# Kernel tuning notes

Hardware: AMD Instinct MI355X
Metric: run time of the kernel (lower is better)

The kernel has to match this reference:

```python
import jax, jax.numpy as jnp
import numpy as np

N_NODES = 50000
N_EDGES = 800000
H = 128
IN_DIM = 512
N_LAYERS = 3
LN_EPS = 1e-5


def setup_inputs() -> dict:
    key = jax.random.key(0)
    ks = jax.random.split(key, 12)
    s_in = 1.0 / np.sqrt(IN_DIM)
    s_h = 1.0 / np.sqrt(H)
    return {
        "peptide_feature": jax.random.normal(ks[0], (N_NODES, IN_DIM), jnp.float32),
        "proj_W": jax.random.uniform(ks[1], (IN_DIM, H), jnp.float32, -s_in, s_in),
        "proj_b": jax.random.uniform(ks[2], (H,), jnp.float32, -s_in, s_in),
        "edge_emb": jax.random.normal(ks[3], (100, H), jnp.float32),
        "conv_W1": jax.random.uniform(ks[4], (N_LAYERS, H, H), jnp.float32, -s_h, s_h),
        "conv_b1": jax.random.uniform(ks[5], (N_LAYERS, H), jnp.float32, -s_h, s_h),
        "conv_W2": jax.random.uniform(ks[6], (N_LAYERS, H, H), jnp.float32, -s_h, s_h),
        "conv_b2": jax.random.uniform(ks[7], (N_LAYERS, H), jnp.float32, -s_h, s_h),
        "ln_gamma": jnp.ones((H,), jnp.float32),
        "ln_beta": jnp.zeros((H,), jnp.float32),
        "edge_index": jax.random.randint(ks[8], (2, N_EDGES), 0, N_NODES, jnp.int64 if jax.config.jax_enable_x64 else jnp.int32),
        "edge_attr": jax.random.randint(ks[9], (N_EDGES, 1), 0, 100, jnp.int64 if jax.config.jax_enable_x64 else jnp.int32),
    }


def reference(peptide_feature, proj_W, proj_b, edge_emb, conv_W1, conv_b1,
              conv_W2, conv_b2, ln_gamma, ln_beta, edge_index, edge_attr):
    # aanet_proj: Linear(512, H)
    x = peptide_feature @ proj_W + proj_b  # [N, H]
    # edge type embedding lookup
    ea = edge_emb[edge_attr[:, 0]]  # [E, H]
    src, dst = edge_index[0], edge_index[1]
    n = x.shape[0]
    for i in range(N_LAYERS):
        # GINEConv (eps=0): aggr_i = sum_{(j->i)} relu(x_j + e_ji); out = MLP(x + aggr)
        msg = jax.nn.relu(x[src] + ea)  # [E, H] gather + add + relu
        agg = jax.ops.segment_sum(msg, dst, num_segments=n)  # scatter-add [N, H]
        h = x + agg
        h = jax.nn.relu(h @ conv_W1[i] + conv_b1[i]) @ conv_W2[i] + conv_b2[i]
        x = h + x  # residual
    # LayerNorm over last dim
    mu = jnp.mean(x, axis=-1, keepdims=True)
    var = jnp.var(x, axis=-1, keepdims=True)
    return ln_gamma * (x - mu) * jax.lax.rsqrt(var + LN_EPS) + ln_beta
```

## Files before the change

kernel.cpp:

```cpp
#include <hip/hip_runtime.h>
#include <hip/hip_bf16.h>

#define N_NODES 50000
#define N_EDGES 800000
#define H 128
#define IN_DIM 512
#define N_LAYERS 3
#define LN_EPS 1e-5f
#define SCAN_B ((N_NODES + 255) / 256)
#define BIN_CH 8192
#define BIN_BLOCKS ((N_EDGES + BIN_CH - 1) / BIN_CH)

typedef __attribute__((ext_vector_type(4))) float f32x4;
typedef __attribute__((ext_vector_type(8))) short short8;

__device__ inline ushort f2bfu(float f) {
    __hip_bfloat16 h = __float2bfloat16(f);
    return __builtin_bit_cast(ushort, h);
}
__device__ inline float bfu2f(ushort u) {
    uint v = ((uint)u) << 16;
    return __builtin_bit_cast(float, v);
}
__device__ inline float lobf(uint u) { return __builtin_bit_cast(float, u << 16); }
__device__ inline float hibf(uint u) { return __builtin_bit_cast(float, u & 0xffff0000u); }

#define SWZ(row, byte) ((byte) ^ (((row) & 7) << 4))

__device__ inline short8 cvt8(float4 a, float4 b) {
    short8 v;
    v[0] = (short)f2bfu(a.x); v[1] = (short)f2bfu(a.y);
    v[2] = (short)f2bfu(a.z); v[3] = (short)f2bfu(a.w);
    v[4] = (short)f2bfu(b.x); v[5] = (short)f2bfu(b.y);
    v[6] = (short)f2bfu(b.z); v[7] = (short)f2bfu(b.w);
    return v;
}


__global__ __launch_bounds__(256) void bucketcnt_k(const int* __restrict__ dst,
                                                   int* __restrict__ bcnt) {
    __shared__ int cnt[SCAN_B];
    int tid = threadIdx.x;
    if (tid < SCAN_B) cnt[tid] = 0;
    __syncthreads();
    int e0 = blockIdx.x * BIN_CH;
    #pragma unroll
    for (int k = 0; k < BIN_CH / 256; k++) {
        int e = e0 + k * 256 + tid;
        if (e < N_EDGES) atomicAdd(&cnt[dst[e] >> 8], 1);
    }
    __syncthreads();
    if (tid < SCAN_B && cnt[tid] > 0) atomicAdd(&bcnt[tid], cnt[tid]);
}

__global__ __launch_bounds__(256) void scanb_k(const int* __restrict__ bcnt,
                                               int* __restrict__ bbase,
                                               int* __restrict__ bcur) {
    __shared__ int s[256];
    int t = threadIdx.x;
    int v = (t < SCAN_B) ? bcnt[t] : 0;
    s[t] = v;
    __syncthreads();
    for (int d = 1; d < 256; d <<= 1) {
        int u = (t >= d) ? s[t - d] : 0;
        __syncthreads();
        s[t] += u;
        __syncthreads();
    }
    int exc = s[t] - v;
    bbase[t] = exc;
    if (t < SCAN_B) bcur[t] = exc;
}


__global__ __launch_bounds__(256) void binpass_k(const int* __restrict__ src,
                                                 const int* __restrict__ dst,
                                                 const int* __restrict__ attr,
                                                 int* __restrict__ bcur,
                                                 int* __restrict__ tmp_ep,
                                                 ushort* __restrict__ tmp_dst) {
    __shared__ int cnt[SCAN_B];
    __shared__ int lofs[SCAN_B];
    __shared__ int gbase[SCAN_B];
    __shared__ int cnt2[SCAN_B];
    __shared__ int scan_s[256];
    __shared__ int stage_ep[BIN_CH];
    __shared__ ushort stage_dst[BIN_CH];
    int tid = threadIdx.x;
    int e0 = blockIdx.x * BIN_CH;

    if (tid < SCAN_B) { cnt[tid] = 0; cnt2[tid] = 0; }
    __syncthreads();

    #pragma unroll
    for (int k = 0; k < BIN_CH / 256; k++) {
        int e = e0 + k * 256 + tid;
        if (e < N_EDGES) atomicAdd(&cnt[dst[e] >> 8], 1);
    }
    __syncthreads();

    int v = (tid < SCAN_B) ? cnt[tid] : 0;
    scan_s[tid] = v;
    __syncthreads();
    for (int d = 1; d < 256; d <<= 1) {
        int u = (tid >= d) ? scan_s[tid - d] : 0;
        __syncthreads();
        scan_s[tid] += u;
        __syncthreads();
    }
    if (tid < SCAN_B) lofs[tid] = scan_s[tid] - v;
    int total = scan_s[255];

    if (tid < SCAN_B && v > 0) gbase[tid] = atomicAdd(&bcur[tid], v);
    __syncthreads();

    #pragma unroll
    for (int k = 0; k < BIN_CH / 256; k++) {
        int e = e0 + k * 256 + tid;
        if (e < N_EDGES) {
            int d = dst[e];
            int b = d >> 8;
            int loc = lofs[b] + atomicAdd(&cnt2[b], 1);
            stage_ep[loc] = src[e] | (attr[e] << 16);
            stage_dst[loc] = (ushort)d;
        }
    }
    __syncthreads();

    for (int i = tid; i < total; i += 256) {
        ushort d = stage_dst[i];
        int b = d >> 8;
        int gp = gbase[b] + (i - lofs[b]);
        tmp_ep[gp] = stage_ep[i];
        tmp_dst[gp] = d;
    }
}


__global__ __launch_bounds__(256) void finepass_k(const int* __restrict__ tmp_ep,
                                                  const ushort* __restrict__ tmp_dst,
                                                  const int* __restrict__ bbase,
                                                  int* __restrict__ offs,
                                                  int* __restrict__ epack) {
    __shared__ int deg[256];
    __shared__ int cur[256];
    __shared__ int wsum[4];
    int tid = threadIdx.x;
    deg[tid] = 0;
    __syncthreads();
    int lo = bbase[blockIdx.x], hi = bbase[blockIdx.x + 1];
    for (int i = lo + tid; i < hi; i += 256)
        atomicAdd(&deg[tmp_dst[i] & 255], 1);
    __syncthreads();
    int lane = tid & 63, w = tid >> 6;
    int v = deg[tid];
    int inc = v;
    #pragma unroll
    for (int d = 1; d < 64; d <<= 1) {
        int u = __shfl_up(inc, d);
        if (lane >= d) inc += u;
    }
    if (lane == 63) wsum[w] = inc;
    __syncthreads();
    int wo = 0;
    #pragma unroll
    for (int k = 0; k < 4; k++) if (k < w) wo += wsum[k];
    int exc = lo + wo + inc - v;
    int node = (blockIdx.x << 8) + tid;
    if (node < N_NODES) offs[node] = exc;
    if (node == N_NODES - 1) offs[N_NODES] = exc + v;
    cur[tid] = exc;
    __syncthreads();
    for (int i = lo + tid; i < hi; i += 256) {
        ushort d = tmp_dst[i];
        int ep = tmp_ep[i];
        int pos = atomicAdd(&cur[d & 255], 1);
        epack[pos] = ep;
    }
}


__global__ __launch_bounds__(256) void prep_w_k(const float* __restrict__ pW,
                                                const float* __restrict__ W1,
                                                const float* __restrict__ W2,
                                                const float* __restrict__ emb,
                                                short* __restrict__ Wt,
                                                short* __restrict__ W1t,
                                                short* __restrict__ W2t,
                                                ushort* __restrict__ embb,
                                                int* __restrict__ bcnt) {
    int i = blockIdx.x * 256 + threadIdx.x;
    if (i < 128 * 512) {
        int n = i >> 9, k = i & 511;
        Wt[i] = (short)f2bfu(pW[k * 128 + n]);
    }
    if (i < 3 * 128 * 128) {
        int l = i >> 14, rem = i & 16383, n = rem >> 7, k = rem & 127;
        W1t[i] = (short)f2bfu(W1[l * 16384 + k * 128 + n]);
        W2t[i] = (short)f2bfu(W2[l * 16384 + k * 128 + n]);
    }
    if (i < 100 * 128) embb[i] = f2bfu(emb[i]);
    if (i < 256) bcnt[i] = 0;
}


__global__ __launch_bounds__(512) void proj_k(const float* __restrict__ pep,
                                              const short* __restrict__ Wt,
                                              const float* __restrict__ b,
                                              float* __restrict__ xf,
                                              ushort* __restrict__ xb) {
    __shared__ short SW[128 * 512];
    int tid = threadIdx.x, lane = tid & 63, wid = tid >> 6;

    #pragma unroll
    for (int c = 0; c < 16; c++) {
        int ch = tid + c * 512;
        int row = ch >> 6, kc = (ch & 63) * 16;
        short8 w = *(const short8*)((const char*)Wt + row * 1024 + kc);
        *(short8*)((char*)SW + SWZ(row, row * 1024 + kc)) = w;
    }
    __syncthreads();

    int m0 = blockIdx.x * 256 + wid * 32;

    const float* arow[2];
    #pragma unroll
    for (int mi = 0; mi < 2; mi++) {
        int node = m0 + mi * 16 + (lane & 15);
        if (node > N_NODES - 1) node = N_NODES - 1;
        arow[mi] = pep + (size_t)node * IN_DIM + ((lane >> 4) << 3);
    }

    f32x4 acc[2][8] = {};
    float4 A[4][2][2];
    #pragma unroll
    for (int d = 0; d < 4; d++)
        #pragma unroll
        for (int mi = 0; mi < 2; mi++) {
            A[d][mi][0] = *(const float4*)(arow[mi] + d * 32);
            A[d][mi][1] = *(const float4*)(arow[mi] + d * 32 + 4);
        }

    #pragma unroll
    for (int ks = 0; ks < 16; ks++) {
        int d = ks & 3;
        short8 af0 = cvt8(A[d][0][0], A[d][0][1]);
        short8 af1 = cvt8(A[d][1][0], A[d][1][1]);
        if (ks + 4 < 16) {
            #pragma unroll
            for (int mi = 0; mi < 2; mi++) {
                A[d][mi][0] = *(const float4*)(arow[mi] + (ks + 4) * 32);
                A[d][mi][1] = *(const float4*)(arow[mi] + (ks + 4) * 32 + 4);
            }
        }
        int kb2 = (ks * 32 + ((lane >> 4) << 3)) * 2;
        #pragma unroll
        for (int ni = 0; ni < 8; ni++) {
            int n = ni * 16 + (lane & 15);
            short8 bf = *(const short8*)((const char*)SW + SWZ(n, n * 1024 + kb2));
            acc[0][ni] = __builtin_amdgcn_mfma_f32_16x16x32_bf16(af0, bf, acc[0][ni], 0, 0, 0);
            acc[1][ni] = __builtin_amdgcn_mfma_f32_16x16x32_bf16(af1, bf, acc[1][ni], 0, 0, 0);
        }
    }

    #pragma unroll
    for (int ni = 0; ni < 8; ni++) {
        int col = ni * 16 + (lane & 15);
        float bb = b[col];
        #pragma unroll
        for (int mi = 0; mi < 2; mi++) {
            int rowb = m0 + mi * 16 + ((lane >> 4) << 2);
            #pragma unroll
            for (int r = 0; r < 4; r++) {
                int node = rowb + r;
                if (node < N_NODES) {
                    float v = acc[mi][ni][r] + bb;
                    xf[(size_t)node * H + col] = v;
                    xb[(size_t)node * H + col] = f2bfu(v);
                }
            }
        }
    }
}


__global__ __launch_bounds__(256) void gather_k(const ushort* __restrict__ xb,
                                                const int* __restrict__ offs,
                                                const int* __restrict__ epack,
                                                const ushort* __restrict__ embb,
                                                ushort* __restrict__ aggb) {
    int node = (blockIdx.x * 256 + threadIdx.x) >> 6;
    int lane = threadIdx.x & 63;
    if (node >= N_NODES) return;
    int beg = offs[node], end = offs[node + 1];
    float ax = 0.f, ay = 0.f;
    for (int base = beg; base < end; base += 64) {
        int myp = (base + lane < end) ? epack[base + lane] : 0;
        int cnt = min(64, end - base);
        int j = 0;
        for (; j + 4 <= cnt; j += 4) {
            int p0 = __shfl(myp, j), p1 = __shfl(myp, j + 1);
            int p2 = __shfl(myp, j + 2), p3 = __shfl(myp, j + 3);
            uint x0 = *(const uint*)(xb + (size_t)(p0 & 0xffff) * H + lane * 2);
            uint e0 = *(const uint*)(embb + (size_t)(p0 >> 16) * H + lane * 2);
            uint x1 = *(const uint*)(xb + (size_t)(p1 & 0xffff) * H + lane * 2);
            uint e1 = *(const uint*)(embb + (size_t)(p1 >> 16) * H + lane * 2);
            uint x2 = *(const uint*)(xb + (size_t)(p2 & 0xffff) * H + lane * 2);
            uint e2 = *(const uint*)(embb + (size_t)(p2 >> 16) * H + lane * 2);
            uint x3 = *(const uint*)(xb + (size_t)(p3 & 0xffff) * H + lane * 2);
            uint e3 = *(const uint*)(embb + (size_t)(p3 >> 16) * H + lane * 2);
            ax += fmaxf(lobf(x0) + lobf(e0), 0.f);
            ay += fmaxf(hibf(x0) + hibf(e0), 0.f);
            ax += fmaxf(lobf(x1) + lobf(e1), 0.f);
            ay += fmaxf(hibf(x1) + hibf(e1), 0.f);
            ax += fmaxf(lobf(x2) + lobf(e2), 0.f);
            ay += fmaxf(hibf(x2) + hibf(e2), 0.f);
            ax += fmaxf(lobf(x3) + lobf(e3), 0.f);
            ay += fmaxf(hibf(x3) + hibf(e3), 0.f);
        }
        for (; j < cnt; j++) {
            int p = __shfl(myp, j);
            uint xv = *(const uint*)(xb + (size_t)(p & 0xffff) * H + lane * 2);
            uint ev = *(const uint*)(embb + (size_t)(p >> 16) * H + lane * 2);
            ax += fmaxf(lobf(xv) + lobf(ev), 0.f);
            ay += fmaxf(hibf(xv) + hibf(ev), 0.f);
        }
    }
    uint packed = (uint)f2bfu(ax) | ((uint)f2bfu(ay) << 16);
    *(uint*)(aggb + (size_t)node * H + lane * 2) = packed;
}


#define MLP_ROWS 64
__global__ __launch_bounds__(256) void mlp_k(float* __restrict__ xf,
                                             ushort* __restrict__ xb,
                                             const ushort* __restrict__ aggb,
                                             const short* __restrict__ W1t,
                                             const float* __restrict__ b1,
                                             const short* __restrict__ W2t,
                                             const float* __restrict__ b2,
                                             const float* __restrict__ gamma,
                                             const float* __restrict__ beta,
                                             float* __restrict__ out,
                                             int write_xb, int do_ln) {
    __shared__ short S[MLP_ROWS * 128];
    __shared__ short Wb[128 * 128];
    int tid = threadIdx.x, lane = tid & 63, wid = tid >> 6;
    int wr = wid >> 1, wc = wid & 1;
    int m0 = blockIdx.x * MLP_ROWS;

    #pragma unroll
    for (int c = 0; c < 4; c++) {
        int ch = tid + c * 256;
        int row = ch >> 4, k8 = (ch & 15) * 8;
        int node = m0 + row;
        short8 hv;
        if (node < N_NODES) {
            const float* xp = xf + (size_t)node * H + k8;
            float4 x0 = *(const float4*)xp;
            float4 x1 = *(const float4*)(xp + 4);
            short8 ag = *(const short8*)(aggb + (size_t)node * H + k8);
            hv[0] = (short)f2bfu(x0.x + bfu2f((ushort)ag[0]));
            hv[1] = (short)f2bfu(x0.y + bfu2f((ushort)ag[1]));
            hv[2] = (short)f2bfu(x0.z + bfu2f((ushort)ag[2]));
            hv[3] = (short)f2bfu(x0.w + bfu2f((ushort)ag[3]));
            hv[4] = (short)f2bfu(x1.x + bfu2f((ushort)ag[4]));
            hv[5] = (short)f2bfu(x1.y + bfu2f((ushort)ag[5]));
            hv[6] = (short)f2bfu(x1.z + bfu2f((ushort)ag[6]));
            hv[7] = (short)f2bfu(x1.w + bfu2f((ushort)ag[7]));
        } else {
            hv = (short8)0;
        }
        *(short8*)((char*)S + SWZ(row, row * 256 + k8 * 2)) = hv;
    }
    #pragma unroll
    for (int c = 0; c < 8; c++) {
        int ch = tid + c * 256;
        int row = ch >> 4, k8 = (ch & 15) * 8;
        short8 w = *(const short8*)(W1t + row * H + k8);
        *(short8*)((char*)Wb + SWZ(row, row * 256 + k8 * 2)) = w;
    }
    short8 wreg2[8];
    #pragma unroll
    for (int c = 0; c < 8; c++) {
        int ch = tid + c * 256;
        int row = ch >> 4, k8 = (ch & 15) * 8;
        wreg2[c] = *(const short8*)(W2t + row * H + k8);
    }
    __syncthreads();

    f32x4 a1[2][4] = {};
    #pragma unroll
    for (int ks = 0; ks < 4; ks++) {
        int kb = ks * 32 + (lane >> 4) * 8;
        short8 af[2], bfr[4];
        #pragma unroll
        for (int mi = 0; mi < 2; mi++) {
            int r = wr * 32 + mi * 16 + (lane & 15);
            af[mi] = *(const short8*)((const char*)S + SWZ(r, r * 256 + kb * 2));
        }
        #pragma unroll
        for (int ni = 0; ni < 4; ni++) {
            int n = wc * 64 + ni * 16 + (lane & 15);
            bfr[ni] = *(const short8*)((const char*)Wb + SWZ(n, n * 256 + kb * 2));
        }
        #pragma unroll
        for (int mi = 0; mi < 2; mi++)
            #pragma unroll
            for (int ni = 0; ni < 4; ni++)
                a1[mi][ni] = __builtin_amdgcn_mfma_f32_16x16x32_bf16(
                    af[mi], bfr[ni], a1[mi][ni], 0, 0, 0);
    }
    __syncthreads();

    #pragma unroll
    for (int ni = 0; ni < 4; ni++) {
        int n = wc * 64 + ni * 16 + (lane & 15);
        float bb = b1[n];
        #pragma unroll
        for (int mi = 0; mi < 2; mi++) {
            int mrow = wr * 32 + mi * 16 + ((lane >> 4) << 2);
            #pragma unroll
            for (int r = 0; r < 4; r++) {
                int m = mrow + r;
                float tv = fmaxf(a1[mi][ni][r] + bb, 0.f);
                *(ushort*)((char*)S + SWZ(m, m * 256 + n * 2)) = f2bfu(tv);
            }
        }
    }
    #pragma unroll
    for (int c = 0; c < 8; c++) {
        int ch = tid + c * 256;
        int row = ch >> 4, k8 = (ch & 15) * 8;
        *(short8*)((char*)Wb + SWZ(row, row * 256 + k8 * 2)) = wreg2[c];
    }
    __syncthreads();

    f32x4 a2[4][2] = {};
    #pragma unroll
    for (int ks = 0; ks < 4; ks++) {
        int kb = ks * 32 + (lane >> 4) * 8;
        short8 af[4], bfr[2];
        #pragma unroll
        for (int mi = 0; mi < 4; mi++) {
            int n2 = wr * 64 + mi * 16 + (lane & 15);
            af[mi] = *(const short8*)((const char*)Wb + SWZ(n2, n2 * 256 + kb * 2));
        }
        #pragma unroll
        for (int ni = 0; ni < 2; ni++) {
            int m = wc * 32 + ni * 16 + (lane & 15);
            bfr[ni] = *(const short8*)((const char*)S + SWZ(m, m * 256 + kb * 2));
        }
        #pragma unroll
        for (int mi = 0; mi < 4; mi++)
            #pragma unroll
            for (int ni = 0; ni < 2; ni++)
                a2[mi][ni] = __builtin_amdgcn_mfma_f32_16x16x32_bf16(
                    af[mi], bfr[ni], a2[mi][ni], 0, 0, 0);
    }

    if (!do_ln) {
        #pragma unroll
        for (int ni = 0; ni < 2; ni++) {
            int node = m0 + wc * 32 + ni * 16 + (lane & 15);
            if (node >= N_NODES) continue;
            #pragma unroll
            for (int mi = 0; mi < 4; mi++) {
                int n2b = wr * 64 + mi * 16 + ((lane >> 4) << 2);
                float4 xo = *(float4*)(xf + (size_t)node * H + n2b);
                float4 bb = *(const float4*)(b2 + n2b);
                float4 o;
                o.x = a2[mi][ni][0] + bb.x + xo.x;
                o.y = a2[mi][ni][1] + bb.y + xo.y;
                o.z = a2[mi][ni][2] + bb.z + xo.z;
                o.w = a2[mi][ni][3] + bb.w + xo.w;
                *(float4*)(xf + (size_t)node * H + n2b) = o;
                if (write_xb) {
                    ushort us[4] = {f2bfu(o.x), f2bfu(o.y), f2bfu(o.z), f2bfu(o.w)};
                    *(ulong*)(xb + (size_t)node * H + n2b) = *(ulong*)us;
                }
            }
        }
    } else {
        float* F = (float*)Wb;
        __syncthreads();
        #pragma unroll
        for (int ni = 0; ni < 2; ni++) {
            int nl = wc * 32 + ni * 16 + (lane & 15);
            int node = m0 + nl;
            #pragma unroll
            for (int mi = 0; mi < 4; mi++) {
                int n2b = wr * 64 + mi * 16 + ((lane >> 4) << 2);
                float4 o = {0.f, 0.f, 0.f, 0.f};
                if (node < N_NODES) {
                    float4 xo = *(float4*)(xf + (size_t)node * H + n2b);
                    float4 bb = *(const float4*)(b2 + n2b);
                    o.x = a2[mi][ni][0] + bb.x + xo.x;
                    o.y = a2[mi][ni][1] + bb.y + xo.y;
                    o.z = a2[mi][ni][2] + bb.z + xo.z;
                    o.w = a2[mi][ni][3] + bb.w + xo.w;
                }
                *(float4*)((char*)F + SWZ(nl, nl * 512 + n2b * 4)) = o;
            }
        }
        __syncthreads();
        float2 gm = ((const float2*)gamma)[lane];
        float2 bt = ((const float2*)beta)[lane];
        for (int i = 0; i < 16; i++) {
            int row = wid * 16 + i;
            int node = m0 + row;
            if (node >= N_NODES) break;
            float2 v = *(float2*)((char*)F + SWZ(row, row * 512 + lane * 8));
            float s = v.x + v.y;
            #pragma unroll
            for (int d = 1; d < 64; d <<= 1) s += __shfl_xor(s, d);
            float mu = s * (1.f / 128.f);
            float dx = v.x - mu, dy = v.y - mu;
            float q = dx * dx + dy * dy;
            #pragma unroll
            for (int d = 1; d < 64; d <<= 1) q += __shfl_xor(q, d);
            float inv = rsqrtf(q * (1.f / 128.f) + LN_EPS);
            float2 o2;
            o2.x = gm.x * dx * inv + bt.x;
            o2.y = gm.y * dy * inv + bt.y;
            ((float2*)(out + (size_t)node * H))[lane] = o2;
        }
    }
}


extern "C" void kernel_launch(void* const* d_in, const int* in_sizes, int n_in,
                              void* d_out, int out_size, void* d_ws, size_t ws_size,
                              hipStream_t stream) {
    const float* pep    = (const float*)d_in[0];
    const float* proj_W = (const float*)d_in[1];
    const float* proj_b = (const float*)d_in[2];
    const float* emb    = (const float*)d_in[3];
    const float* cW1    = (const float*)d_in[4];
    const float* cb1    = (const float*)d_in[5];
    const float* cW2    = (const float*)d_in[6];
    const float* cb2    = (const float*)d_in[7];
    const float* gamma  = (const float*)d_in[8];
    const float* beta   = (const float*)d_in[9];
    const int*   eidx   = (const int*)d_in[10];
    const int*   attr   = (const int*)d_in[11];
    const int* src = eidx;
    const int* dst = eidx + N_EDGES;

    char* w = (char*)d_ws;
    float*  xf    = (float*)w;              w += (size_t)N_NODES * H * 4;
    ushort* xb    = (ushort*)w;             w += (size_t)N_NODES * H * 2;
    ushort* aggb  = (ushort*)w;             w += (size_t)N_NODES * H * 2;
    short*  Wt    = (short*)w;              w += 128 * 512 * 2;
    short*  W1t   = (short*)w;              w += 3 * 128 * 128 * 2;
    short*  W2t   = (short*)w;              w += 3 * 128 * 128 * 2;
    ushort* embb  = (ushort*)w;             w += 100 * 128 * 2;
    int*    offs  = (int*)w;                w += (N_NODES + 16) * 4;
    int*    bcnt  = (int*)w;                w += 256 * 4;
    int*    bbase = (int*)w;                w += 260 * 4;
    int*    bcur  = (int*)w;                w += 256 * 4;
    int*    epack = (int*)w;                w += (size_t)N_EDGES * 4;
    int*    tmp_ep = (int*)w;               w += (size_t)N_EDGES * 4;
    ushort* tmp_dst = (ushort*)w;           w += (size_t)N_EDGES * 2;

    float* out = (float*)d_out;

    prep_w_k<<<256, 256, 0, stream>>>(proj_W, cW1, cW2, emb, Wt, W1t, W2t, embb, bcnt);
    bucketcnt_k<<<BIN_BLOCKS, 256, 0, stream>>>(dst, bcnt);
    scanb_k<<<1, 256, 0, stream>>>(bcnt, bbase, bcur);
    binpass_k<<<BIN_BLOCKS, 256, 0, stream>>>(src, dst, attr, bcur, tmp_ep, tmp_dst);
    finepass_k<<<SCAN_B, 256, 0, stream>>>(tmp_ep, tmp_dst, bbase, offs, epack);

    proj_k<<<(N_NODES + 255) / 256, 512, 0, stream>>>(pep, Wt, proj_b, xf, xb);

    for (int l = 0; l < N_LAYERS; l++) {
        gather_k<<<(N_NODES * 64 + 255) / 256, 256, 0, stream>>>(
            xb, offs, epack, embb, aggb);
        mlp_k<<<(N_NODES + MLP_ROWS - 1) / MLP_ROWS, 256, 0, stream>>>(
            xf, xb, aggb,
            W1t + (size_t)l * H * H, cb1 + (size_t)l * H,
            W2t + (size_t)l * H * H, cb2 + (size_t)l * H,
            gamma, beta, out,
            (l < N_LAYERS - 1) ? 1 : 0,
            (l == N_LAYERS - 1) ? 1 : 0);
    }
}
```

Before: 277.4 us.

## Fuse CSR build into one persistent kernel with grid barriers, unroll gather

```diff
diff --git a/kernel.cpp b/kernel.cpp
--- a/kernel.cpp
+++ b/kernel.cpp
@@ -8,8 +8,7 @@
 #define N_LAYERS 3
 #define LN_EPS 1e-5f
 #define SCAN_B ((N_NODES + 255) / 256)
-#define BIN_CH 8192
-#define BIN_BLOCKS ((N_EDGES + BIN_CH - 1) / BIN_CH)
+#define CSR_CH 4096
 
 typedef __attribute__((ext_vector_type(4))) float f32x4;
 typedef __attribute__((ext_vector_type(8))) short short8;
@@ -36,147 +35,15 @@
     return v;
 }
 
-
-__global__ __launch_bounds__(256) void bucketcnt_k(const int* __restrict__ dst,
-                                                   int* __restrict__ bcnt) {
-    __shared__ int cnt[SCAN_B];
-    int tid = threadIdx.x;
-    if (tid < SCAN_B) cnt[tid] = 0;
-    __syncthreads();
-    int e0 = blockIdx.x * BIN_CH;
-    #pragma unroll
-    for (int k = 0; k < BIN_CH / 256; k++) {
-        int e = e0 + k * 256 + tid;
-        if (e < N_EDGES) atomicAdd(&cnt[dst[e] >> 8], 1);
-    }
-    __syncthreads();
-    if (tid < SCAN_B && cnt[tid] > 0) atomicAdd(&bcnt[tid], cnt[tid]);
-}
-
-__global__ __launch_bounds__(256) void scanb_k(const int* __restrict__ bcnt,
-                                               int* __restrict__ bbase,
-                                               int* __restrict__ bcur) {
-    __shared__ int s[256];
-    int t = threadIdx.x;
-    int v = (t < SCAN_B) ? bcnt[t] : 0;
-    s[t] = v;
-    __syncthreads();
-    for (int d = 1; d < 256; d <<= 1) {
-        int u = (t >= d) ? s[t - d] : 0;
-        __syncthreads();
-        s[t] += u;
-        __syncthreads();
-    }
-    int exc = s[t] - v;
-    bbase[t] = exc;
-    if (t < SCAN_B) bcur[t] = exc;
-}
-
-
-__global__ __launch_bounds__(256) void binpass_k(const int* __restrict__ src,
-                                                 const int* __restrict__ dst,
-                                                 const int* __restrict__ attr,
-                                                 int* __restrict__ bcur,
-                                                 int* __restrict__ tmp_ep,
-                                                 ushort* __restrict__ tmp_dst) {
-    __shared__ int cnt[SCAN_B];
-    __shared__ int lofs[SCAN_B];
-    __shared__ int gbase[SCAN_B];
-    __shared__ int cnt2[SCAN_B];
-    __shared__ int scan_s[256];
-    __shared__ int stage_ep[BIN_CH];
-    __shared__ ushort stage_dst[BIN_CH];
-    int tid = threadIdx.x;
-    int e0 = blockIdx.x * BIN_CH;
-
-    if (tid < SCAN_B) { cnt[tid] = 0; cnt2[tid] = 0; }
-    __syncthreads();
-
-    #pragma unroll
-    for (int k = 0; k < BIN_CH / 256; k++) {
-        int e = e0 + k * 256 + tid;
-        if (e < N_EDGES) atomicAdd(&cnt[dst[e] >> 8], 1);
-    }
-    __syncthreads();
-
-    int v = (tid < SCAN_B) ? cnt[tid] : 0;
-    scan_s[tid] = v;
-    __syncthreads();
-    for (int d = 1; d < 256; d <<= 1) {
-        int u = (tid >= d) ? scan_s[tid - d] : 0;
-        __syncthreads();
-        scan_s[tid] += u;
-        __syncthreads();
-    }
-    if (tid < SCAN_B) lofs[tid] = scan_s[tid] - v;
-    int total = scan_s[255];
-
-    if (tid < SCAN_B && v > 0) gbase[tid] = atomicAdd(&bcur[tid], v);
-    __syncthreads();
-
-    #pragma unroll
-    for (int k = 0; k < BIN_CH / 256; k++) {
-        int e = e0 + k * 256 + tid;
-        if (e < N_EDGES) {
-            int d = dst[e];
-            int b = d >> 8;
-            int loc = lofs[b] + atomicAdd(&cnt2[b], 1);
-            stage_ep[loc] = src[e] | (attr[e] << 16);
-            stage_dst[loc] = (ushort)d;
-        }
-    }
-    __syncthreads();
-
-    for (int i = tid; i < total; i += 256) {
-        ushort d = stage_dst[i];
-        int b = d >> 8;
-        int gp = gbase[b] + (i - lofs[b]);
-        tmp_ep[gp] = stage_ep[i];
-        tmp_dst[gp] = d;
-    }
-}
-
-
-__global__ __launch_bounds__(256) void finepass_k(const int* __restrict__ tmp_ep,
-                                                  const ushort* __restrict__ tmp_dst,
-                                                  const int* __restrict__ bbase,
-                                                  int* __restrict__ offs,
-                                                  int* __restrict__ epack) {
-    __shared__ int deg[256];
-    __shared__ int cur[256];
-    __shared__ int wsum[4];
-    int tid = threadIdx.x;
-    deg[tid] = 0;
-    __syncthreads();
-    int lo = bbase[blockIdx.x], hi = bbase[blockIdx.x + 1];
-    for (int i = lo + tid; i < hi; i += 256)
-        atomicAdd(&deg[tmp_dst[i] & 255], 1);
-    __syncthreads();
-    int lane = tid & 63, w = tid >> 6;
-    int v = deg[tid];
-    int inc = v;
-    #pragma unroll
-    for (int d = 1; d < 64; d <<= 1) {
-        int u = __shfl_up(inc, d);
-        if (lane >= d) inc += u;
-    }
-    if (lane == 63) wsum[w] = inc;
-    __syncthreads();
-    int wo = 0;
-    #pragma unroll
-    for (int k = 0; k < 4; k++) if (k < w) wo += wsum[k];
-    int exc = lo + wo + inc - v;
-    int node = (blockIdx.x << 8) + tid;
-    if (node < N_NODES) offs[node] = exc;
-    if (node == N_NODES - 1) offs[N_NODES] = exc + v;
-    cur[tid] = exc;
-    __syncthreads();
-    for (int i = lo + tid; i < hi; i += 256) {
-        ushort d = tmp_dst[i];
-        int ep = tmp_ep[i];
-        int pos = atomicAdd(&cur[d & 255], 1);
-        epack[pos] = ep;
-    }
+__device__ inline void gbar(int* ctr, int target) {
+    __syncthreads();
+    if (threadIdx.x == 0) {
+        __threadfence();
+        atomicAdd(ctr, 1);
+        while (atomicAdd(ctr, 0) < target) {}
+        __threadfence();
+    }
+    __syncthreads();
 }
 
 
@@ -188,7 +55,9 @@
                                                 short* __restrict__ W1t,
                                                 short* __restrict__ W2t,
                                                 ushort* __restrict__ embb,
-                                                int* __restrict__ bcnt) {
+                                                int* __restrict__ bcnt,
+                                                int* __restrict__ bdelta,
+                                                int* __restrict__ barctr) {
     int i = blockIdx.x * 256 + threadIdx.x;
     if (i < 128 * 512) {
         int n = i >> 9, k = i & 511;
@@ -200,7 +69,127 @@
         W2t[i] = (short)f2bfu(W2[l * 16384 + k * 128 + n]);
     }
     if (i < 100 * 128) embb[i] = f2bfu(emb[i]);
-    if (i < 256) bcnt[i] = 0;
+    if (i < 256) { bcnt[i] = 0; bdelta[i] = 0; }
+    if (i == 0) *barctr = 0;
+}
+
+
+__global__ __launch_bounds__(256) void csr_k(const int* __restrict__ src,
+                                             const int* __restrict__ dst,
+                                             const int* __restrict__ attr,
+                                             int* __restrict__ bcnt,
+                                             int* __restrict__ bdelta,
+                                             int* __restrict__ barctr,
+                                             int* __restrict__ gtmp_ep,
+                                             ushort* __restrict__ gtmp_dst,
+                                             int* __restrict__ offs,
+                                             int* __restrict__ epack) {
+    __shared__ int hist[SCAN_B];
+    __shared__ int scan_s[256];
+    __shared__ int sbase[257];
+    __shared__ int lofs[SCAN_B];
+    __shared__ int gbase[SCAN_B];
+    __shared__ int cnt2[SCAN_B];
+    __shared__ int wsum[4];
+    __shared__ int stage_ep[CSR_CH];
+    __shared__ ushort stage_dst[CSR_CH];
+    int tid = threadIdx.x, bid = blockIdx.x;
+    int e0 = bid * CSR_CH;
+
+    if (tid < SCAN_B) hist[tid] = 0;
+    __syncthreads();
+    #pragma unroll
+    for (int k = 0; k < CSR_CH / 256; k++) {
+        int e = e0 + k * 256 + tid;
+        if (e < N_EDGES) atomicAdd(&hist[dst[e] >> 8], 1);
+    }
+    __syncthreads();
+    if (tid < SCAN_B && hist[tid] > 0) atomicAdd(&bcnt[tid], hist[tid]);
+    gbar(barctr, SCAN_B);
+
+    int v = (tid < SCAN_B) ? bcnt[tid] : 0;
+    scan_s[tid] = v;
+    __syncthreads();
+    for (int d = 1; d < 256; d <<= 1) {
+        int u = (tid >= d) ? scan_s[tid - d] : 0;
+        __syncthreads();
+        scan_s[tid] += u;
+        __syncthreads();
+    }
+    sbase[tid] = scan_s[tid] - v;
+    __syncthreads();
+
+    int lv = (tid < SCAN_B) ? hist[tid] : 0;
+    scan_s[tid] = lv;
+    __syncthreads();
+    for (int d = 1; d < 256; d <<= 1) {
+        int u = (tid >= d) ? scan_s[tid - d] : 0;
+        __syncthreads();
+        scan_s[tid] += u;
+        __syncthreads();
+    }
+    if (tid < SCAN_B) {
+        lofs[tid] = scan_s[tid] - lv;
+        cnt2[tid] = 0;
+        if (lv > 0) gbase[tid] = sbase[tid] + atomicAdd(&bdelta[tid], lv);
+    }
+    int total = scan_s[255];
+    __syncthreads();
+    #pragma unroll
+    for (int k = 0; k < CSR_CH / 256; k++) {
+        int e = e0 + k * 256 + tid;
+        if (e < N_EDGES) {
+            int d = dst[e];
+            int b = d >> 8;
+            int loc = lofs[b] + atomicAdd(&cnt2[b], 1);
+            stage_ep[loc] = src[e] | (attr[e] << 16);
+            stage_dst[loc] = (ushort)d;
+        }
+    }
+    __syncthreads();
+    for (int i = tid; i < total; i += 256) {
+        ushort d = stage_dst[i];
+        int b = d >> 8;
+        int gp = gbase[b] + (i - lofs[b]);
+        gtmp_ep[gp] = stage_ep[i];
+        gtmp_dst[gp] = d;
+    }
+    gbar(barctr, 2 * SCAN_B);
+
+    int lo = sbase[bid], hi = sbase[bid + 1];
+    __syncthreads();
+    int* deg = scan_s;
+    int* cur = stage_ep;
+    deg[tid] = 0;
+    __syncthreads();
+    for (int i = lo + tid; i < hi; i += 256)
+        atomicAdd(&deg[gtmp_dst[i] & 255], 1);
+    __syncthreads();
+    int lane = tid & 63, w = tid >> 6;
+    int dv = deg[tid];
+    int inc = dv;
+    #pragma unroll
+    for (int d = 1; d < 64; d <<= 1) {
+        int u = __shfl_up(inc, d);
+        if (lane >= d) inc += u;
+    }
+    if (lane == 63) wsum[w] = inc;
+    __syncthreads();
+    int wo = 0;
+    #pragma unroll
+    for (int k = 0; k < 4; k++) if (k < w) wo += wsum[k];
+    int exc = lo + wo + inc - dv;
+    int node = (bid << 8) + tid;
+    if (node < N_NODES) offs[node] = exc;
+    if (node == N_NODES - 1) offs[N_NODES] = exc + dv;
+    cur[tid] = exc;
+    __syncthreads();
+    for (int i = lo + tid; i < hi; i += 256) {
+        ushort d = gtmp_dst[i];
+        int ep = gtmp_ep[i];
+        int pos = atomicAdd(&cur[d & 255], 1);
+        epack[pos] = ep;
+    }
 }
 
 
@@ -298,6 +287,36 @@
         int myp = (base + lane < end) ? epack[base + lane] : 0;
         int cnt = min(64, end - base);
         int j = 0;
+        for (; j + 8 <= cnt; j += 8) {
+            int p0 = __shfl(myp, j),     p1 = __shfl(myp, j + 1);
+            int p2 = __shfl(myp, j + 2), p3 = __shfl(myp, j + 3);
+            int p4 = __shfl(myp, j + 4), p5 = __shfl(myp, j + 5);
+            int p6 = __shfl(myp, j + 6), p7 = __shfl(myp, j + 7);
+            uint x0 = *(const uint*)(xb + (size_t)(p0 & 0xffff) * H + lane * 2);
+            uint e0 = *(const uint*)(embb + (size_t)(p0 >> 16) * H + lane * 2);
+            uint x1 = *(const uint*)(xb + (size_t)(p1 & 0xffff) * H + lane * 2);
+            uint e1 = *(const uint*)(embb + (size_t)(p1 >> 16) * H + lane * 2);
+            uint x2 = *(const uint*)(xb + (size_t)(p2 & 0xffff) * H + lane * 2);
+            uint e2 = *(const uint*)(embb + (size_t)(p2 >> 16) * H + lane * 2);
+            uint x3 = *(const uint*)(xb + (size_t)(p3 & 0xffff) * H + lane * 2);
+            uint e3 = *(const uint*)(embb + (size_t)(p3 >> 16) * H + lane * 2);
+            uint x4 = *(const uint*)(xb + (size_t)(p4 & 0xffff) * H + lane * 2);
+            uint e4 = *(const uint*)(embb + (size_t)(p4 >> 16) * H + lane * 2);
+            uint x5 = *(const uint*)(xb + (size_t)(p5 & 0xffff) * H + lane * 2);
+            uint e5 = *(const uint*)(embb + (size_t)(p5 >> 16) * H + lane * 2);
+            uint x6 = *(const uint*)(xb + (size_t)(p6 & 0xffff) * H + lane * 2);
+            uint e6 = *(const uint*)(embb + (size_t)(p6 >> 16) * H + lane * 2);
+            uint x7 = *(const uint*)(xb + (size_t)(p7 & 0xffff) * H + lane * 2);
+            uint e7 = *(const uint*)(embb + (size_t)(p7 >> 16) * H + lane * 2);
+            ax += fmaxf(lobf(x0) + lobf(e0), 0.f); ay += fmaxf(hibf(x0) + hibf(e0), 0.f);
+            ax += fmaxf(lobf(x1) + lobf(e1), 0.f); ay += fmaxf(hibf(x1) + hibf(e1), 0.f);
+            ax += fmaxf(lobf(x2) + lobf(e2), 0.f); ay += fmaxf(hibf(x2) + hibf(e2), 0.f);
+            ax += fmaxf(lobf(x3) + lobf(e3), 0.f); ay += fmaxf(hibf(x3) + hibf(e3), 0.f);
+            ax += fmaxf(lobf(x4) + lobf(e4), 0.f); ay += fmaxf(hibf(x4) + hibf(e4), 0.f);
+            ax += fmaxf(lobf(x5) + lobf(e5), 0.f); ay += fmaxf(hibf(x5) + hibf(e5), 0.f);
+            ax += fmaxf(lobf(x6) + lobf(e6), 0.f); ay += fmaxf(hibf(x6) + hibf(e6), 0.f);
+            ax += fmaxf(lobf(x7) + lobf(e7), 0.f); ay += fmaxf(hibf(x7) + hibf(e7), 0.f);
+        }
         for (; j + 4 <= cnt; j += 4) {
             int p0 = __shfl(myp, j), p1 = __shfl(myp, j + 1);
             int p2 = __shfl(myp, j + 2), p3 = __shfl(myp, j + 3);
@@ -309,14 +328,10 @@
             uint e2 = *(const uint*)(embb + (size_t)(p2 >> 16) * H + lane * 2);
             uint x3 = *(const uint*)(xb + (size_t)(p3 & 0xffff) * H + lane * 2);
             uint e3 = *(const uint*)(embb + (size_t)(p3 >> 16) * H + lane * 2);
-            ax += fmaxf(lobf(x0) + lobf(e0), 0.f);
-            ay += fmaxf(hibf(x0) + hibf(e0), 0.f);
-            ax += fmaxf(lobf(x1) + lobf(e1), 0.f);
-            ay += fmaxf(hibf(x1) + hibf(e1), 0.f);
-            ax += fmaxf(lobf(x2) + lobf(e2), 0.f);
-            ay += fmaxf(hibf(x2) + hibf(e2), 0.f);
-            ax += fmaxf(lobf(x3) + lobf(e3), 0.f);
-            ay += fmaxf(hibf(x3) + hibf(e3), 0.f);
+            ax += fmaxf(lobf(x0) + lobf(e0), 0.f); ay += fmaxf(hibf(x0) + hibf(e0), 0.f);
+            ax += fmaxf(lobf(x1) + lobf(e1), 0.f); ay += fmaxf(hibf(x1) + hibf(e1), 0.f);
+            ax += fmaxf(lobf(x2) + lobf(e2), 0.f); ay += fmaxf(hibf(x2) + hibf(e2), 0.f);
+            ax += fmaxf(lobf(x3) + lobf(e3), 0.f); ay += fmaxf(hibf(x3) + hibf(e3), 0.f);
         }
         for (; j < cnt; j++) {
             int p = __shfl(myp, j);
@@ -356,18 +371,11 @@
         int node = m0 + row;
         short8 hv;
         if (node < N_NODES) {
-            const float* xp = xf + (size_t)node * H + k8;
-            float4 x0 = *(const float4*)xp;
-            float4 x1 = *(const float4*)(xp + 4);
+            short8 xv = *(const short8*)(xb + (size_t)node * H + k8);
             short8 ag = *(const short8*)(aggb + (size_t)node * H + k8);
-            hv[0] = (short)f2bfu(x0.x + bfu2f((ushort)ag[0]));
-            hv[1] = (short)f2bfu(x0.y + bfu2f((ushort)ag[1]));
-            hv[2] = (short)f2bfu(x0.z + bfu2f((ushort)ag[2]));
-            hv[3] = (short)f2bfu(x0.w + bfu2f((ushort)ag[3]));
-            hv[4] = (short)f2bfu(x1.x + bfu2f((ushort)ag[4]));
-            hv[5] = (short)f2bfu(x1.y + bfu2f((ushort)ag[5]));
-            hv[6] = (short)f2bfu(x1.z + bfu2f((ushort)ag[6]));
-            hv[7] = (short)f2bfu(x1.w + bfu2f((ushort)ag[7]));
+            #pragma unroll
+            for (int q = 0; q < 8; q++)
+                hv[q] = (short)f2bfu(bfu2f((ushort)xv[q]) + bfu2f((ushort)ag[q]));
         } else {
             hv = (short8)0;
         }
@@ -548,28 +556,27 @@
     const int* dst = eidx + N_EDGES;
 
     char* w = (char*)d_ws;
-    float*  xf    = (float*)w;              w += (size_t)N_NODES * H * 4;
-    ushort* xb    = (ushort*)w;             w += (size_t)N_NODES * H * 2;
-    ushort* aggb  = (ushort*)w;             w += (size_t)N_NODES * H * 2;
-    short*  Wt    = (short*)w;              w += 128 * 512 * 2;
-    short*  W1t   = (short*)w;              w += 3 * 128 * 128 * 2;
-    short*  W2t   = (short*)w;              w += 3 * 128 * 128 * 2;
-    ushort* embb  = (ushort*)w;             w += 100 * 128 * 2;
-    int*    offs  = (int*)w;                w += (N_NODES + 16) * 4;
-    int*    bcnt  = (int*)w;                w += 256 * 4;
-    int*    bbase = (int*)w;                w += 260 * 4;
-    int*    bcur  = (int*)w;                w += 256 * 4;
-    int*    epack = (int*)w;                w += (size_t)N_EDGES * 4;
+    float*  xf     = (float*)w;             w += (size_t)N_NODES * H * 4;
+    ushort* xb     = (ushort*)w;            w += (size_t)N_NODES * H * 2;
+    ushort* aggb   = (ushort*)w;            w += (size_t)N_NODES * H * 2;
+    short*  Wt     = (short*)w;             w += 128 * 512 * 2;
+    short*  W1t    = (short*)w;             w += 3 * 128 * 128 * 2;
+    short*  W2t    = (short*)w;             w += 3 * 128 * 128 * 2;
+    ushort* embb   = (ushort*)w;            w += 100 * 128 * 2;
+    int*    offs   = (int*)w;               w += (N_NODES + 16) * 4;
+    int*    bcnt   = (int*)w;               w += 256 * 4;
+    int*    bdelta = (int*)w;               w += 256 * 4;
+    int*    barctr = (int*)w;               w += 16 * 4;
+    int*    epack  = (int*)w;               w += (size_t)N_EDGES * 4;
     int*    tmp_ep = (int*)w;               w += (size_t)N_EDGES * 4;
     ushort* tmp_dst = (ushort*)w;           w += (size_t)N_EDGES * 2;
 
     float* out = (float*)d_out;
 
-    prep_w_k<<<256, 256, 0, stream>>>(proj_W, cW1, cW2, emb, Wt, W1t, W2t, embb, bcnt);
-    bucketcnt_k<<<BIN_BLOCKS, 256, 0, stream>>>(dst, bcnt);
-    scanb_k<<<1, 256, 0, stream>>>(bcnt, bbase, bcur);
-    binpass_k<<<BIN_BLOCKS, 256, 0, stream>>>(src, dst, attr, bcur, tmp_ep, tmp_dst);
-    finepass_k<<<SCAN_B, 256, 0, stream>>>(tmp_ep, tmp_dst, bbase, offs, epack);
+    prep_w_k<<<256, 256, 0, stream>>>(proj_W, cW1, cW2, emb, Wt, W1t, W2t, embb,
+                                      bcnt, bdelta, barctr);
+    csr_k<<<SCAN_B, 256, 0, stream>>>(src, dst, attr, bcnt, bdelta, barctr,
+                                      tmp_ep, tmp_dst, offs, epack);
 
     proj_k<<<(N_NODES + 255) / 256, 512, 0, stream>>>(pep, Wt, proj_b, xf, xb);
 
```

New measurement: 280.4 us. About the same (+1.1%).
